# Optimization experiments

Measured on AMD Instinct MI355X. Metric: run time of the kernel, lower is better.

## Reference

```python
import jax, jax.numpy as jnp
import numpy as np

N_NODES = 32
GAT_OUT = 64
LSTM_H = 128
N_CLS = 4
NEG_SLOPE = 0.2


def setup_inputs() -> dict:
    key = jax.random.key(0)
    ks = jax.random.split(key, 12)
    B, T, E = 32, 512, 96
    F, H = GAT_OUT, LSTM_H
    s = 0.05
    return {
        "x_seq": jax.random.normal(ks[0], (B, T, N_NODES), jnp.float32),
        "edge_index": jax.random.randint(ks[1], (2, E), 0, N_NODES, jnp.int32),
        # GATConv params (heads=1): lin weight [in=1, F], attention vectors [F], bias [F]
        "w_gat": jax.random.normal(ks[2], (1, F), jnp.float32) * s,
        "att_src": jax.random.normal(ks[3], (F,), jnp.float32) * s,
        "att_dst": jax.random.normal(ks[4], (F,), jnp.float32) * s,
        "b_gat": jnp.zeros((F,), jnp.float32),
        # LSTM params, torch gate order (i, f, g, o)
        "W_ih": jax.random.normal(ks[5], (N_NODES * F, 4 * H), jnp.float32) * s,
        "W_hh": jax.random.normal(ks[6], (H, 4 * H), jnp.float32) * s,
        "b_ih": jnp.zeros((4 * H,), jnp.float32),
        "b_hh": jnp.zeros((4 * H,), jnp.float32),
        # classifier
        "W_fc": jax.random.normal(ks[7], (H, N_CLS), jnp.float32) * s,
        "b_fc": jnp.zeros((N_CLS,), jnp.float32),
    }


def _forward(x_seq, edge_index, w_gat, att_src, att_dst, b_gat,
             W_ih, W_hh, b_ih, b_hh, W_fc, b_fc):
    B, T, N = x_seq.shape
    F = w_gat.shape[1]
    H = W_hh.shape[0]

    # --- GAT over all (B,T) steps at once (PyG GATConv, heads=1, self-loops) ---
    loops = jnp.arange(N, dtype=edge_index.dtype)
    src = jnp.concatenate([edge_index[0], loops])  # [Et]
    dst = jnp.concatenate([edge_index[1], loops])  # [Et]
    Et = src.shape[0]

    h = x_seq[..., None] * w_gat            # [B,T,N,F] (in_channels=1 linear)
    a_s = h @ att_src                        # [B,T,N]
    a_d = h @ att_dst                        # [B,T,N]
    e = a_s[..., src] + a_d[..., dst]        # [B,T,Et]
    e = jnp.where(e > 0, e, NEG_SLOPE * e)   # LeakyReLU(0.2)

    # segment softmax over destination node, batched over B*T
    e2 = jnp.moveaxis(e, -1, 0).reshape(Et, B * T)
    m = jax.ops.segment_max(e2, dst, num_segments=N)        # [N,B*T]
    ex = jnp.exp(e2 - m[dst])
    z = jax.ops.segment_sum(ex, dst, num_segments=N)        # [N,B*T]
    alpha = ex / z[dst]                                      # [Et,B*T]
    alpha = jnp.moveaxis(alpha.reshape(Et, B, T), 0, -1)     # [B,T,Et]

    msg = alpha[..., None] * h[:, :, src, :]                 # [B,T,Et,F]
    onehot = (dst[:, None] == jnp.arange(N)).astype(h.dtype)  # [Et,N]
    out = jnp.einsum('btef,en->btnf', msg, onehot) + b_gat    # [B,T,N,F]

    seq = out.reshape(B, T, N * F)           # [B,T,2048]

    # --- single-layer LSTM (batch_first), torch gate order i,f,g,o ---
    xw = seq @ W_ih + (b_ih + b_hh)          # [B,T,4H]

    def step(carry, xw_t):
        hs, cs = carry
        g = xw_t + hs @ W_hh                 # [B,4H]
        i, f, gg, o = jnp.split(g, 4, axis=-1)
        cs = jax.nn.sigmoid(f) * cs + jax.nn.sigmoid(i) * jnp.tanh(gg)
        hs = jax.nn.sigmoid(o) * jnp.tanh(cs)
        return (hs, cs), None

    h0 = jnp.zeros((B, H), seq.dtype)
    (h_last, _), _ = jax.lax.scan(step, (h0, h0), jnp.moveaxis(xw, 1, 0))

    return h_last @ W_fc + b_fc              # [B,num_classes]


def reference(x_seq, edge_index, w_gat, att_src, att_dst, b_gat,
              W_ih, W_hh, b_ih, b_hh, W_fc, b_fc):
    return _forward(x_seq, edge_index, w_gat, att_src, att_dst, b_gat,
                    W_ih, W_hh, b_ih, b_hh, W_fc, b_fc)
```

## Files before the change

### kernel.cpp

```cpp
#include <hip/hip_runtime.h>

#define NN 32
#define FF 64
#define HH 128
#define G4 512
#define BB 32
#define TT 512
#define ET 128
#define NPOS (BB*TT)

__device__ __forceinline__ float frcp(float x) { return __builtin_amdgcn_rcpf(x); }

__global__ __launch_bounds__(512) void prep_kernel(const float* __restrict__ w_gat,
                                                   const float* __restrict__ b_gat,
                                                   const float* __restrict__ W_ih,
                                                   const float* __restrict__ W_hh,
                                                   float* __restrict__ W_eff,
                                                   float* __restrict__ biasp,
                                                   float* __restrict__ Wt) {
  int j = threadIdx.x;
  int n = blockIdx.x;
  float accw = 0.f, accb = 0.f;
#pragma unroll 8
  for (int f = 0; f < FF; ++f) {
    float wv = W_ih[(n * FF + f) * G4 + j];
    accw = fmaf(w_gat[f], wv, accw);
    accb = fmaf(b_gat[f], wv, accb);
  }
  W_eff[n * G4 + j] = accw;
  biasp[n * G4 + j] = accb;
  int g0 = (n * G4 + j) * 4;
#pragma unroll
  for (int q = 0; q < 4; ++q) {
    int E = g0 + q;
    int tl = E >> 7;
    int idx = E & 127;
    int s = idx >> 5;
    int jj = (idx >> 3) & 3;
    int g = (idx >> 1) & 3;
    int e = idx & 1;
    int r = tl >> 2, kq = tl & 3, lr = r & 3;
    int bb = (lr - s) & 3;
    int k = kq * 32 + 8 * bb + 2 * jj + e;
    Wt[E] = W_hh[k * G4 + g * 128 + r];
  }
}

__global__ __launch_bounds__(256) void gatxw_kernel(const float* __restrict__ x_seq,
                                                    const int* __restrict__ ei,
                                                    const float* __restrict__ w_gat,
                                                    const float* __restrict__ att_src,
                                                    const float* __restrict__ att_dst,
                                                    const float* __restrict__ b_ih,
                                                    const float* __restrict__ b_hh,
                                                    const float* __restrict__ W_eff,
                                                    const float* __restrict__ biasp,
                                                    float* __restrict__ xw) {
  __shared__ int srt[ET];
  __shared__ int offs[NN + 1];
  __shared__ int cnt[NN];
  __shared__ float xs[256];
  __shared__ float sl[256];
  __shared__ float scal_sh[2];
  int tid = threadIdx.x;
  int posbase = blockIdx.x * 8;
  float we0[NN], we1[NN];
#pragma unroll
  for (int nn = 0; nn < NN; ++nn) {
    we0[nn] = W_eff[nn * G4 + tid];
    we1[nn] = W_eff[nn * G4 + 256 + tid];
  }
  float b0 = b_ih[tid] + b_hh[tid];
  float b1 = b_ih[256 + tid] + b_hh[256 + tid];
#pragma unroll 8
  for (int n = 0; n < NN; ++n) {
    b0 += biasp[n * G4 + tid];
    b1 += biasp[n * G4 + 256 + tid];
  }
  if (tid < NN) cnt[tid] = 0;
  __syncthreads();
  int es = 0, ed = 0, tk = 0;
  if (tid < ET) {
    if (tid < 96) { es = ei[tid]; ed = ei[96 + tid]; }
    else { es = tid - 96; ed = tid - 96; }
    tk = atomicAdd(&cnt[ed], 1);
  }
  __syncthreads();
  if (tid == 0) {
    offs[0] = 0;
    for (int n = 0; n < NN; ++n) offs[n + 1] = offs[n] + cnt[n];
  }
  if (tid == 1) {
    float cs = 0.f, cd = 0.f;
    for (int f = 0; f < FF; ++f) {
      cs = fmaf(w_gat[f], att_src[f], cs);
      cd = fmaf(w_gat[f], att_dst[f], cd);
    }
    scal_sh[0] = cs;
    scal_sh[1] = cd;
  }
  __syncthreads();
  if (tid < ET) srt[offs[ed] + tk] = es;
  xs[tid] = x_seq[posbase * NN + tid];
  __syncthreads();
  float cs = scal_sh[0], cd = scal_sh[1];
  int p = tid >> 5, n = tid & 31;
  int base = p * 32;
  int e0 = offs[n], e1 = offs[n + 1];
  float xn = xs[base + n];
  float cdxn = cd * xn;
  float m = -3.0e38f;
  for (int e = e0; e < e1; ++e) {
    float ev = fmaf(cs, xs[base + srt[e]], cdxn);
    ev = ev > 0.f ? ev : 0.2f * ev;
    m = fmaxf(m, ev);
  }
  float z = 0.f, sa = 0.f;
  for (int e = e0; e < e1; ++e) {
    float xsv = xs[base + srt[e]];
    float ev = fmaf(cs, xsv, cdxn);
    ev = ev > 0.f ? ev : 0.2f * ev;
    float ex = __expf(ev - m);
    z += ex;
    sa = fmaf(ex, xsv, sa);
  }
  sl[p * 32 + n] = sa * frcp(z);
  __syncthreads();
  for (int pp = 0; pp < 8; ++pp) {
    const float4* sp = (const float4*)&sl[pp * 32];
    float a0 = b0, a1 = b1;
#pragma unroll
    for (int q = 0; q < 8; ++q) {
      float4 sv = sp[q];
      a0 = fmaf(sv.x, we0[4 * q], a0);
      a0 = fmaf(sv.y, we0[4 * q + 1], a0);
      a0 = fmaf(sv.z, we0[4 * q + 2], a0);
      a0 = fmaf(sv.w, we0[4 * q + 3], a0);
      a1 = fmaf(sv.x, we1[4 * q], a1);
      a1 = fmaf(sv.y, we1[4 * q + 1], a1);
      a1 = fmaf(sv.z, we1[4 * q + 2], a1);
      a1 = fmaf(sv.w, we1[4 * q + 3], a1);
    }
    size_t row = (size_t)(posbase + pp) * G4;
    xw[row + tid] = a0;
    xw[row + 256 + tid] = a1;
  }
}


#define PK4F(HP, W0, W1, W2, W3) \
  "v_pk_fma_f32 v[216:217], v[" HP "], v[" W0 "], 0\n\t" \
  "v_pk_fma_f32 v[218:219], v[" HP "], v[" W1 "], 0\n\t" \
  "v_pk_fma_f32 v[220:221], v[" HP "], v[" W2 "], 0\n\t" \
  "v_pk_fma_f32 v[222:223], v[" HP "], v[" W3 "], 0\n\t"

#define PK4A(HP, W0, W1, W2, W3) \
  "v_pk_fma_f32 v[216:217], v[" HP "], v[" W0 "], v[216:217]\n\t" \
  "v_pk_fma_f32 v[218:219], v[" HP "], v[" W1 "], v[218:219]\n\t" \
  "v_pk_fma_f32 v[220:221], v[" HP "], v[" W2 "], v[220:221]\n\t" \
  "v_pk_fma_f32 v[222:223], v[" HP "], v[" W3 "], v[222:223]\n\t"

#define ROT8 \
  "v_mov_b32_dpp v32, v32 row_ror:4 row_mask:0xf bank_mask:0xf\n\t" \
  "v_mov_b32_dpp v33, v33 row_ror:4 row_mask:0xf bank_mask:0xf\n\t" \
  "v_mov_b32_dpp v34, v34 row_ror:4 row_mask:0xf bank_mask:0xf\n\t" \
  "v_mov_b32_dpp v35, v35 row_ror:4 row_mask:0xf bank_mask:0xf\n\t" \
  "v_mov_b32_dpp v36, v36 row_ror:4 row_mask:0xf bank_mask:0xf\n\t" \
  "v_mov_b32_dpp v37, v37 row_ror:4 row_mask:0xf bank_mask:0xf\n\t" \
  "v_mov_b32_dpp v38, v38 row_ror:4 row_mask:0xf bank_mask:0xf\n\t" \
  "v_mov_b32_dpp v39, v39 row_ror:4 row_mask:0xf bank_mask:0xf\n\t"

#define PHASE(XSLOT, RD, WR) \
  "ds_read_b128 v[32:35], " RD "\n\t" \
  "ds_read_b128 v[36:39], " RD " offset:16\n\t" \
  "s_waitcnt lgkmcnt(1)\n\t" \
  PK4F("32:33", "64:65",   "66:67",   "68:69",   "70:71") \
  PK4A("34:35", "72:73",   "74:75",   "76:77",   "78:79") \
  "s_waitcnt lgkmcnt(0)\n\t" \
  PK4A("36:37", "80:81",   "82:83",   "84:85",   "86:87") \
  PK4A("38:39", "88:89",   "90:91",   "92:93",   "94:95") \
  ROT8 \
  PK4A("32:33", "96:97",   "98:99",   "100:101", "102:103") \
  PK4A("34:35", "104:105", "106:107", "108:109", "110:111") \
  PK4A("36:37", "112:113", "114:115", "116:117", "118:119") \
  PK4A("38:39", "120:121", "122:123", "124:125", "126:127") \
  ROT8 \
  PK4A("32:33", "128:129", "130:131", "132:133", "134:135") \
  PK4A("34:35", "136:137", "138:139", "140:141", "142:143") \
  PK4A("36:37", "144:145", "146:147", "148:149", "150:151") \
  PK4A("38:39", "152:153", "154:155", "156:157", "158:159") \
  ROT8 \
  PK4A("32:33", "160:161", "162:163", "164:165", "166:167") \
  PK4A("34:35", "168:169", "170:171", "172:173", "174:175") \
  PK4A("36:37", "176:177", "178:179", "180:181", "182:183") \
  PK4A("38:39", "184:185", "186:187", "188:189", "190:191") \
  "s_waitcnt vmcnt(3)\n\t" \
  "v_mov_b32 v215, " XSLOT "\n\t" \
  "global_load_dword " XSLOT ", v194, %[xwb]\n\t" \
  "v_add_u32 v194, 0x800, v194\n\t" \
  "v_add_f32 v204, v216, v217\n\t" \
  "v_add_f32 v205, v218, v219\n\t" \
  "v_add_f32 v206, v220, v221\n\t" \
  "v_add_f32 v207, v222, v223\n\t" \
  "v_add_f32_dpp v204, v204, v204 quad_perm:[1,0,3,2] row_mask:0xf bank_mask:0xf\n\t" \
  "v_add_f32_dpp v205, v205, v205 quad_perm:[1,0,3,2] row_mask:0xf bank_mask:0xf\n\t" \
  "v_add_f32_dpp v206, v206, v206 quad_perm:[1,0,3,2] row_mask:0xf bank_mask:0xf\n\t" \
  "v_add_f32_dpp v207, v207, v207 quad_perm:[1,0,3,2] row_mask:0xf bank_mask:0xf\n\t" \
  "v_add_f32_dpp v204, v204, v204 quad_perm:[2,3,0,1] row_mask:0xf bank_mask:0xf\n\t" \
  "v_add_f32_dpp v205, v205, v205 quad_perm:[2,3,0,1] row_mask:0xf bank_mask:0xf\n\t" \
  "v_add_f32_dpp v206, v206, v206 quad_perm:[2,3,0,1] row_mask:0xf bank_mask:0xf\n\t" \
  "v_add_f32_dpp v207, v207, v207 quad_perm:[2,3,0,1] row_mask:0xf bank_mask:0xf\n\t" \
  "v_cndmask_b32 v208, v204, v205, s[22:23]\n\t" \
  "v_cndmask_b32 v209, v206, v207, s[22:23]\n\t" \
  "v_cndmask_b32 v208, v208, v209, s[24:25]\n\t" \
  "v_add_f32 v208, v208, v215\n\t" \
  "v_mul_f32 v209, v200, v208\n\t" \
  "v_exp_f32 v209, v209\n\t" \
  "s_nop 0\n\t" \
  "v_add_f32 v209, 1.0, v209\n\t" \
  "v_rcp_f32 v209, v209\n\t" \
  "s_nop 0\n\t" \
  "v_fma_f32 v210, v201, v209, v202\n\t" \
  "s_nop 1\n\t" \
  "v_add_f32_dpp v211, v210, v203 quad_perm:[0,0,0,0] row_mask:0xf bank_mask:0xf\n\t" \
  "v_add_f32_dpp v212, v210, v203 quad_perm:[1,1,1,1] row_mask:0xf bank_mask:0xf\n\t" \
  "v_add_f32_dpp v213, v210, v203 quad_perm:[2,2,2,2] row_mask:0xf bank_mask:0xf\n\t" \
  "v_add_f32_dpp v214, v210, v203 quad_perm:[3,3,3,3] row_mask:0xf bank_mask:0xf\n\t" \
  "v_mul_f32 v211, v211, v213\n\t" \
  "v_fma_f32 v199, v212, v199, v211\n\t" \
  "v_mul_f32 v209, 0x4038aa3b, v199\n\t" \
  "v_exp_f32 v209, v209\n\t" \
  "s_nop 0\n\t" \
  "v_add_f32 v209, 1.0, v209\n\t" \
  "v_rcp_f32 v209, v209\n\t" \
  "s_nop 0\n\t" \
  "v_fma_f32 v209, -2.0, v209, 1.0\n\t" \
  "v_mul_f32 v209, v214, v209\n\t" \
  "ds_write_b32 " WR ", v209\n\t" \
  "s_waitcnt lgkmcnt(0)\n\t" \
  "s_barrier\n\t"

__global__ __launch_bounds__(512, 2) void lstm_kernel(const float* __restrict__ xw,
                                                      const float* __restrict__ Wt,
                                                      const float* __restrict__ W_fc,
                                                      const float* __restrict__ b_fc,
                                                      float* __restrict__ out) {
  __shared__ __align__(16) float lds[256];
  int b = blockIdx.x, tid = threadIdx.x;
  int r = tid >> 2, kq = tid & 3;
  int lr = r & 3;
  if (tid < 256) lds[tid] = 0.f;
  const float* xwb = xw + (size_t)b * TT * G4;
  unsigned xoff0 = (unsigned)((kq * 128 + r) * 4);
  unsigned wtoff = (unsigned)(tid * 512);
  unsigned lbase = (unsigned)(uintptr_t)&lds[0];
  unsigned rda = lbase + (unsigned)(kq * 128 + lr * 32);
  unsigned rdb = rda + 512;
  unsigned wra = lbase + (unsigned)(r * 4);
  unsigned wrb = wra + 512;
  float kmulf = (kq == 2) ? __uint_as_float(0x4038aa3bu)
                          : __uint_as_float(0xbfb8aa3bu);
  float Af = (kq == 2) ? -2.f : 1.f;
  float Bf = (kq == 2) ? 1.f : 0.f;
  unsigned kqodd = kq & 1, kqhi = kq >> 1;
  __syncthreads();
  asm volatile(
    "v_mov_b32 v194, %[xo]\n\t"
    "v_mov_b32 v195, %[rda]\n\t"
    "v_mov_b32 v196, %[rdb]\n\t"
    "v_mov_b32 v197, %[wra]\n\t"
    "v_mov_b32 v198, %[wrb]\n\t"
    "v_mov_b32 v199, 0\n\t"
    "v_mov_b32 v200, %[km]\n\t"
    "v_mov_b32 v201, %[Aa]\n\t"
    "v_mov_b32 v202, %[Bb]\n\t"
    "v_mov_b32 v203, 0\n\t"
    "v_cmp_eq_u32 s[22:23], 1, %[kodd]\n\t"
    "v_cmp_eq_u32 s[24:25], 1, %[khi]\n\t"
    "global_load_dword v224, v194, %[xwb]\n\t"
    "v_add_u32 v194, 0x800, v194\n\t"
    "global_load_dword v225, v194, %[xwb]\n\t"
    "v_add_u32 v194, 0x800, v194\n\t"
    "global_load_dword v226, v194, %[xwb]\n\t"
    "v_add_u32 v194, 0x800, v194\n\t"
    "global_load_dword v227, v194, %[xwb]\n\t"
    "v_add_u32 v194, 0x800, v194\n\t"
    "global_load_dwordx4 v[64:67], %[wto], %[wtb] offset:0\n\t"
    "global_load_dwordx4 v[68:71], %[wto], %[wtb] offset:16\n\t"
    "global_load_dwordx4 v[72:75], %[wto], %[wtb] offset:32\n\t"
    "global_load_dwordx4 v[76:79], %[wto], %[wtb] offset:48\n\t"
    "global_load_dwordx4 v[80:83], %[wto], %[wtb] offset:64\n\t"
    "global_load_dwordx4 v[84:87], %[wto], %[wtb] offset:80\n\t"
    "global_load_dwordx4 v[88:91], %[wto], %[wtb] offset:96\n\t"
    "global_load_dwordx4 v[92:95], %[wto], %[wtb] offset:112\n\t"
    "global_load_dwordx4 v[96:99], %[wto], %[wtb] offset:128\n\t"
    "global_load_dwordx4 v[100:103], %[wto], %[wtb] offset:144\n\t"
    "global_load_dwordx4 v[104:107], %[wto], %[wtb] offset:160\n\t"
    "global_load_dwordx4 v[108:111], %[wto], %[wtb] offset:176\n\t"
    "global_load_dwordx4 v[112:115], %[wto], %[wtb] offset:192\n\t"
    "global_load_dwordx4 v[116:119], %[wto], %[wtb] offset:208\n\t"
    "global_load_dwordx4 v[120:123], %[wto], %[wtb] offset:224\n\t"
    "global_load_dwordx4 v[124:127], %[wto], %[wtb] offset:240\n\t"
    "global_load_dwordx4 v[128:131], %[wto], %[wtb] offset:256\n\t"
    "global_load_dwordx4 v[132:135], %[wto], %[wtb] offset:272\n\t"
    "global_load_dwordx4 v[136:139], %[wto], %[wtb] offset:288\n\t"
    "global_load_dwordx4 v[140:143], %[wto], %[wtb] offset:304\n\t"
    "global_load_dwordx4 v[144:147], %[wto], %[wtb] offset:320\n\t"
    "global_load_dwordx4 v[148:151], %[wto], %[wtb] offset:336\n\t"
    "global_load_dwordx4 v[152:155], %[wto], %[wtb] offset:352\n\t"
    "global_load_dwordx4 v[156:159], %[wto], %[wtb] offset:368\n\t"
    "global_load_dwordx4 v[160:163], %[wto], %[wtb] offset:384\n\t"
    "global_load_dwordx4 v[164:167], %[wto], %[wtb] offset:400\n\t"
    "global_load_dwordx4 v[168:171], %[wto], %[wtb] offset:416\n\t"
    "global_load_dwordx4 v[172:175], %[wto], %[wtb] offset:432\n\t"
    "global_load_dwordx4 v[176:179], %[wto], %[wtb] offset:448\n\t"
    "global_load_dwordx4 v[180:183], %[wto], %[wtb] offset:464\n\t"
    "global_load_dwordx4 v[184:187], %[wto], %[wtb] offset:480\n\t"
    "global_load_dwordx4 v[188:191], %[wto], %[wtb] offset:496\n\t"
    "s_waitcnt vmcnt(0)\n\t"
    "s_movk_i32 s20, 0x80\n\t"
    "L_lstm_%=:\n\t"
    PHASE("v224", "v195", "v198")
    PHASE("v225", "v196", "v197")
    PHASE("v226", "v195", "v198")
    PHASE("v227", "v196", "v197")
    "s_sub_u32 s20, s20, 1\n\t"
    "s_cmp_lg_u32 s20, 0\n\t"
    "s_cbranch_scc1 L_lstm_%=\n\t"
    "s_waitcnt vmcnt(0) lgkmcnt(0)\n\t"
    :
    : [xwb]"s"(xwb), [wtb]"s"(Wt), [wto]"v"(wtoff), [xo]"v"(xoff0),
      [rda]"v"(rda), [rdb]"v"(rdb), [wra]"v"(wra), [wrb]"v"(wrb),
      [km]"v"(kmulf), [Aa]"v"(Af), [Bb]"v"(Bf),
      [kodd]"v"(kqodd), [khi]"v"(kqhi)
    : "memory", "scc", "s20", "s22", "s23", "s24", "s25",
      "v32","v33","v34","v35","v36","v37","v38","v39",
      "v40","v41","v42","v43","v44","v45","v46","v47",
      "v48","v49","v50","v51","v52","v53","v54","v55",
      "v56","v57","v58","v59","v60","v61","v62","v63",
      "v64","v65","v66","v67","v68","v69","v70","v71",
      "v72","v73","v74","v75","v76","v77","v78","v79",
      "v80","v81","v82","v83","v84","v85","v86","v87",
      "v88","v89","v90","v91","v92","v93","v94","v95",
      "v96","v97","v98","v99","v100","v101","v102","v103",
      "v104","v105","v106","v107","v108","v109","v110","v111",
      "v112","v113","v114","v115","v116","v117","v118","v119",
      "v120","v121","v122","v123","v124","v125","v126","v127",
      "v128","v129","v130","v131","v132","v133","v134","v135",
      "v136","v137","v138","v139","v140","v141","v142","v143",
      "v144","v145","v146","v147","v148","v149","v150","v151",
      "v152","v153","v154","v155","v156","v157","v158","v159",
      "v160","v161","v162","v163","v164","v165","v166","v167",
      "v168","v169","v170","v171","v172","v173","v174","v175",
      "v176","v177","v178","v179","v180","v181","v182","v183",
      "v184","v185","v186","v187","v188","v189","v190","v191",
      "v192","v193","v194","v195","v196","v197","v198","v199",
      "v200","v201","v202","v203","v204","v205","v206","v207",
      "v208","v209","v210","v211","v212","v213","v214","v215",
      "v216","v217","v218","v219","v220","v221","v222","v223",
      "v224","v225","v226","v227");
  __syncthreads();
  if (tid < 4) {
    float acc = b_fc[tid];
#pragma unroll 8
    for (int k = 0; k < HH; ++k)
      acc = fmaf(lds[k], W_fc[k * 4 + tid], acc);
    out[b * 4 + tid] = acc;
  }
}

extern "C" void kernel_launch(void* const* d_in, const int* in_sizes, int n_in,
                              void* d_out, int out_size, void* d_ws, size_t ws_size,
                              hipStream_t stream) {
  const float* x_seq   = (const float*)d_in[0];
  const int*   ei      = (const int*)d_in[1];
  const float* w_gat   = (const float*)d_in[2];
  const float* att_src = (const float*)d_in[3];
  const float* att_dst = (const float*)d_in[4];
  const float* b_gat   = (const float*)d_in[5];
  const float* W_ih    = (const float*)d_in[6];
  const float* W_hh    = (const float*)d_in[7];
  const float* b_ih    = (const float*)d_in[8];
  const float* b_hh    = (const float*)d_in[9];
  const float* W_fc    = (const float*)d_in[10];
  const float* b_fc    = (const float*)d_in[11];

  float* ws = (float*)d_ws;
  float* Wt    = ws;
  float* xw    = Wt + 65536;
  float* W_eff = xw + (size_t)(NPOS + 8) * G4;
  float* biasp = W_eff + NN * G4;

  prep_kernel<<<NN, G4, 0, stream>>>(w_gat, b_gat, W_ih, W_hh, W_eff, biasp, Wt);
  gatxw_kernel<<<NPOS / 8, 256, 0, stream>>>(x_seq, ei, w_gat, att_src, att_dst,
                                             b_ih, b_hh, W_eff, biasp, xw);
  lstm_kernel<<<BB, 512, 0, stream>>>(xw, Wt, W_fc, b_fc, (float*)d_out);
}
```

Measured before the change: 412.4 us.

## Split LSTM recurrence across 1024 threads with 8-way k-split per hidden unit

The LSTM kernel moves from 512 to 1024 threads per batch row. Each hidden unit's gate dot products are now split over 8 lanes of 16 k each instead of 4 lanes of 32. This halves the per-thread W_hh register footprint and the FMA chain per step, and replaces the DPP rotation scheme with direct LDS reads at fixed offsets. An extra row_half_mirror reduction stage is added. Gate activation now uses the same sigmoid/tanh trick with the lane-select done via shared multipliers. The cost is more waves per barrier, an added reduction step and redundant activation work per lane group.

```diff
diff --git a/kernel.cpp b/kernel.cpp
--- a/kernel.cpp
+++ b/kernel.cpp
@@ -31,17 +31,16 @@
   biasp[n * G4 + j] = accb;
   int g0 = (n * G4 + j) * 4;
 #pragma unroll
-  for (int q = 0; q < 4; ++q) {
-    int E = g0 + q;
-    int tl = E >> 7;
-    int idx = E & 127;
-    int s = idx >> 5;
-    int jj = (idx >> 3) & 3;
+  for (int qq = 0; qq < 4; ++qq) {
+    int E = g0 + qq;
+    int tl = E >> 6;
+    int idx = E & 63;
+    int cn = idx >> 4;
+    int p = (idx >> 3) & 1;
     int g = (idx >> 1) & 3;
     int e = idx & 1;
-    int r = tl >> 2, kq = tl & 3, lr = r & 3;
-    int bb = (lr - s) & 3;
-    int k = kq * 32 + 8 * bb + 2 * jj + e;
+    int r = tl >> 3, q = tl & 7;
+    int k = q * 16 + 4 * cn + 2 * p + e;
     Wt[E] = W_hh[k * G4 + g * 128 + r];
   }
 }
@@ -149,190 +148,147 @@
 
 
 #define PK4F(HP, W0, W1, W2, W3) \
-  "v_pk_fma_f32 v[216:217], v[" HP "], v[" W0 "], 0\n\t" \
-  "v_pk_fma_f32 v[218:219], v[" HP "], v[" W1 "], 0\n\t" \
-  "v_pk_fma_f32 v[220:221], v[" HP "], v[" W2 "], 0\n\t" \
-  "v_pk_fma_f32 v[222:223], v[" HP "], v[" W3 "], 0\n\t"
+  "v_pk_fma_f32 v[104:105], v[" HP "], v[" W0 "], 0\n\t" \
+  "v_pk_fma_f32 v[106:107], v[" HP "], v[" W1 "], 0\n\t" \
+  "v_pk_fma_f32 v[108:109], v[" HP "], v[" W2 "], 0\n\t" \
+  "v_pk_fma_f32 v[110:111], v[" HP "], v[" W3 "], 0\n\t"
 
 #define PK4A(HP, W0, W1, W2, W3) \
-  "v_pk_fma_f32 v[216:217], v[" HP "], v[" W0 "], v[216:217]\n\t" \
-  "v_pk_fma_f32 v[218:219], v[" HP "], v[" W1 "], v[218:219]\n\t" \
-  "v_pk_fma_f32 v[220:221], v[" HP "], v[" W2 "], v[220:221]\n\t" \
-  "v_pk_fma_f32 v[222:223], v[" HP "], v[" W3 "], v[222:223]\n\t"
-
-#define ROT8 \
-  "v_mov_b32_dpp v32, v32 row_ror:4 row_mask:0xf bank_mask:0xf\n\t" \
-  "v_mov_b32_dpp v33, v33 row_ror:4 row_mask:0xf bank_mask:0xf\n\t" \
-  "v_mov_b32_dpp v34, v34 row_ror:4 row_mask:0xf bank_mask:0xf\n\t" \
-  "v_mov_b32_dpp v35, v35 row_ror:4 row_mask:0xf bank_mask:0xf\n\t" \
-  "v_mov_b32_dpp v36, v36 row_ror:4 row_mask:0xf bank_mask:0xf\n\t" \
-  "v_mov_b32_dpp v37, v37 row_ror:4 row_mask:0xf bank_mask:0xf\n\t" \
-  "v_mov_b32_dpp v38, v38 row_ror:4 row_mask:0xf bank_mask:0xf\n\t" \
-  "v_mov_b32_dpp v39, v39 row_ror:4 row_mask:0xf bank_mask:0xf\n\t"
-
-#define PHASE(XSLOT, RD, WR) \
-  "ds_read_b128 v[32:35], " RD "\n\t" \
-  "ds_read_b128 v[36:39], " RD " offset:16\n\t" \
+  "v_pk_fma_f32 v[104:105], v[" HP "], v[" W0 "], v[104:105]\n\t" \
+  "v_pk_fma_f32 v[106:107], v[" HP "], v[" W1 "], v[106:107]\n\t" \
+  "v_pk_fma_f32 v[108:109], v[" HP "], v[" W2 "], v[108:109]\n\t" \
+  "v_pk_fma_f32 v[110:111], v[" HP "], v[" W3 "], v[110:111]\n\t"
+
+#define PHASE(XSLOT, O0, O1, O2, O3, WOFF) \
+  "ds_read_b128 v[32:35], v124 offset:" O0 "\n\t" \
+  "ds_read_b128 v[36:39], v124 offset:" O1 "\n\t" \
   "s_waitcnt lgkmcnt(1)\n\t" \
-  PK4F("32:33", "64:65",   "66:67",   "68:69",   "70:71") \
-  PK4A("34:35", "72:73",   "74:75",   "76:77",   "78:79") \
+  PK4F("32:33", "40:41", "42:43", "44:45", "46:47") \
+  PK4A("34:35", "48:49", "50:51", "52:53", "54:55") \
+  "ds_read_b128 v[32:35], v124 offset:" O2 "\n\t" \
+  "s_waitcnt lgkmcnt(1)\n\t" \
+  PK4A("36:37", "56:57", "58:59", "60:61", "62:63") \
+  PK4A("38:39", "64:65", "66:67", "68:69", "70:71") \
+  "ds_read_b128 v[36:39], v124 offset:" O3 "\n\t" \
+  "s_waitcnt lgkmcnt(1)\n\t" \
+  PK4A("32:33", "72:73", "74:75", "76:77", "78:79") \
+  PK4A("34:35", "80:81", "82:83", "84:85", "86:87") \
   "s_waitcnt lgkmcnt(0)\n\t" \
-  PK4A("36:37", "80:81",   "82:83",   "84:85",   "86:87") \
-  PK4A("38:39", "88:89",   "90:91",   "92:93",   "94:95") \
-  ROT8 \
-  PK4A("32:33", "96:97",   "98:99",   "100:101", "102:103") \
-  PK4A("34:35", "104:105", "106:107", "108:109", "110:111") \
-  PK4A("36:37", "112:113", "114:115", "116:117", "118:119") \
-  PK4A("38:39", "120:121", "122:123", "124:125", "126:127") \
-  ROT8 \
-  PK4A("32:33", "128:129", "130:131", "132:133", "134:135") \
-  PK4A("34:35", "136:137", "138:139", "140:141", "142:143") \
-  PK4A("36:37", "144:145", "146:147", "148:149", "150:151") \
-  PK4A("38:39", "152:153", "154:155", "156:157", "158:159") \
-  ROT8 \
-  PK4A("32:33", "160:161", "162:163", "164:165", "166:167") \
-  PK4A("34:35", "168:169", "170:171", "172:173", "174:175") \
-  PK4A("36:37", "176:177", "178:179", "180:181", "182:183") \
-  PK4A("38:39", "184:185", "186:187", "188:189", "190:191") \
-  "s_waitcnt vmcnt(3)\n\t" \
-  "v_mov_b32 v215, " XSLOT "\n\t" \
-  "global_load_dword " XSLOT ", v194, %[xwb]\n\t" \
-  "v_add_u32 v194, 0x800, v194\n\t" \
-  "v_add_f32 v204, v216, v217\n\t" \
-  "v_add_f32 v205, v218, v219\n\t" \
-  "v_add_f32 v206, v220, v221\n\t" \
-  "v_add_f32 v207, v222, v223\n\t" \
-  "v_add_f32_dpp v204, v204, v204 quad_perm:[1,0,3,2] row_mask:0xf bank_mask:0xf\n\t" \
-  "v_add_f32_dpp v205, v205, v205 quad_perm:[1,0,3,2] row_mask:0xf bank_mask:0xf\n\t" \
-  "v_add_f32_dpp v206, v206, v206 quad_perm:[1,0,3,2] row_mask:0xf bank_mask:0xf\n\t" \
-  "v_add_f32_dpp v207, v207, v207 quad_perm:[1,0,3,2] row_mask:0xf bank_mask:0xf\n\t" \
-  "v_add_f32_dpp v204, v204, v204 quad_perm:[2,3,0,1] row_mask:0xf bank_mask:0xf\n\t" \
-  "v_add_f32_dpp v205, v205, v205 quad_perm:[2,3,0,1] row_mask:0xf bank_mask:0xf\n\t" \
-  "v_add_f32_dpp v206, v206, v206 quad_perm:[2,3,0,1] row_mask:0xf bank_mask:0xf\n\t" \
-  "v_add_f32_dpp v207, v207, v207 quad_perm:[2,3,0,1] row_mask:0xf bank_mask:0xf\n\t" \
-  "v_cndmask_b32 v208, v204, v205, s[22:23]\n\t" \
-  "v_cndmask_b32 v209, v206, v207, s[22:23]\n\t" \
-  "v_cndmask_b32 v208, v208, v209, s[24:25]\n\t" \
-  "v_add_f32 v208, v208, v215\n\t" \
-  "v_mul_f32 v209, v200, v208\n\t" \
-  "v_exp_f32 v209, v209\n\t" \
+  PK4A("36:37", "88:89", "90:91", "92:93", "94:95") \
+  PK4A("38:39", "96:97", "98:99", "100:101", "102:103") \
+  "v_add_f32 v112, v104, v105\n\t" \
+  "v_add_f32 v113, v106, v107\n\t" \
+  "v_add_f32 v114, v108, v109\n\t" \
+  "v_add_f32 v115, v110, v111\n\t" \
+  "v_add_f32_dpp v112, v112, v112 quad_perm:[1,0,3,2] row_mask:0xf bank_mask:0xf\n\t" \
+  "v_add_f32_dpp v113, v113, v113 quad_perm:[1,0,3,2] row_mask:0xf bank_mask:0xf\n\t" \
+  "v_add_f32_dpp v114, v114, v114 quad_perm:[1,0,3,2] row_mask:0xf bank_mask:0xf\n\t" \
+  "v_add_f32_dpp v115, v115, v115 quad_perm:[1,0,3,2] row_mask:0xf bank_mask:0xf\n\t" \
+  "v_add_f32_dpp v112, v112, v112 quad_perm:[2,3,0,1] row_mask:0xf bank_mask:0xf\n\t" \
+  "v_add_f32_dpp v113, v113, v113 quad_perm:[2,3,0,1] row_mask:0xf bank_mask:0xf\n\t" \
+  "v_add_f32_dpp v114, v114, v114 quad_perm:[2,3,0,1] row_mask:0xf bank_mask:0xf\n\t" \
+  "v_add_f32_dpp v115, v115, v115 quad_perm:[2,3,0,1] row_mask:0xf bank_mask:0xf\n\t" \
+  "v_add_f32_dpp v112, v112, v112 row_half_mirror row_mask:0xf bank_mask:0xf\n\t" \
+  "v_add_f32_dpp v113, v113, v113 row_half_mirror row_mask:0xf bank_mask:0xf\n\t" \
+  "v_add_f32_dpp v114, v114, v114 row_half_mirror row_mask:0xf bank_mask:0xf\n\t" \
+  "v_add_f32_dpp v115, v115, v115 row_half_mirror row_mask:0xf bank_mask:0xf\n\t" \
+  "v_cndmask_b32 v116, v112, v113, s[22:23]\n\t" \
+  "v_cndmask_b32 v117, v114, v115, s[22:23]\n\t" \
+  "v_cndmask_b32 v116, v116, v117, s[24:25]\n\t" \
+  "s_waitcnt vmcnt(1)\n\t" \
+  "v_add_f32 v116, v116, " XSLOT "\n\t" \
+  "global_load_dword " XSLOT ", v123, %[xwb]\n\t" \
+  "v_add_u32 v123, 0x800, v123\n\t" \
+  "v_mul_f32 v117, 0xbfb8aa3b, v116\n\t" \
+  "v_mul_f32 v117, v126, v117\n\t" \
+  "v_exp_f32 v117, v117\n\t" \
   "s_nop 0\n\t" \
-  "v_add_f32 v209, 1.0, v209\n\t" \
-  "v_rcp_f32 v209, v209\n\t" \
+  "v_add_f32 v117, 1.0, v117\n\t" \
+  "v_rcp_f32 v117, v117\n\t" \
   "s_nop 0\n\t" \
-  "v_fma_f32 v210, v201, v209, v202\n\t" \
+  "v_fma_f32 v118, v126, v117, v127\n\t" \
   "s_nop 1\n\t" \
-  "v_add_f32_dpp v211, v210, v203 quad_perm:[0,0,0,0] row_mask:0xf bank_mask:0xf\n\t" \
-  "v_add_f32_dpp v212, v210, v203 quad_perm:[1,1,1,1] row_mask:0xf bank_mask:0xf\n\t" \
-  "v_add_f32_dpp v213, v210, v203 quad_perm:[2,2,2,2] row_mask:0xf bank_mask:0xf\n\t" \
-  "v_add_f32_dpp v214, v210, v203 quad_perm:[3,3,3,3] row_mask:0xf bank_mask:0xf\n\t" \
-  "v_mul_f32 v211, v211, v213\n\t" \
-  "v_fma_f32 v199, v212, v199, v211\n\t" \
-  "v_mul_f32 v209, 0x4038aa3b, v199\n\t" \
-  "v_exp_f32 v209, v209\n\t" \
+  "v_mov_b32_dpp v112, v118 quad_perm:[0,0,0,0] row_mask:0xf bank_mask:0xf\n\t" \
+  "v_mov_b32_dpp v113, v118 quad_perm:[1,1,1,1] row_mask:0xf bank_mask:0xf\n\t" \
+  "v_mov_b32_dpp v114, v118 quad_perm:[2,2,2,2] row_mask:0xf bank_mask:0xf\n\t" \
+  "v_mov_b32_dpp v115, v118 quad_perm:[3,3,3,3] row_mask:0xf bank_mask:0xf\n\t" \
+  "v_mul_f32 v112, v112, v114\n\t" \
+  "v_fma_f32 v120, v113, v120, v112\n\t" \
+  "v_mul_f32 v117, 0x4038aa3b, v120\n\t" \
+  "v_exp_f32 v117, v117\n\t" \
   "s_nop 0\n\t" \
-  "v_add_f32 v209, 1.0, v209\n\t" \
-  "v_rcp_f32 v209, v209\n\t" \
+  "v_add_f32 v117, 1.0, v117\n\t" \
+  "v_rcp_f32 v117, v117\n\t" \
   "s_nop 0\n\t" \
-  "v_fma_f32 v209, -2.0, v209, 1.0\n\t" \
-  "v_mul_f32 v209, v214, v209\n\t" \
-  "ds_write_b32 " WR ", v209\n\t" \
+  "v_fma_f32 v117, -2.0, v117, 1.0\n\t" \
+  "v_mul_f32 v118, v115, v117\n\t" \
+  "ds_write_b32 v125, v118 offset:" WOFF "\n\t" \
   "s_waitcnt lgkmcnt(0)\n\t" \
   "s_barrier\n\t"
 
-__global__ __launch_bounds__(512, 2) void lstm_kernel(const float* __restrict__ xw,
-                                                      const float* __restrict__ Wt,
-                                                      const float* __restrict__ W_fc,
-                                                      const float* __restrict__ b_fc,
-                                                      float* __restrict__ out) {
+__global__ __launch_bounds__(1024, 4) void lstm_kernel(const float* __restrict__ xw,
+                                                       const float* __restrict__ Wt,
+                                                       const float* __restrict__ W_fc,
+                                                       const float* __restrict__ b_fc,
+                                                       float* __restrict__ out) {
   __shared__ __align__(16) float lds[256];
   int b = blockIdx.x, tid = threadIdx.x;
-  int r = tid >> 2, kq = tid & 3;
-  int lr = r & 3;
+  int r = tid >> 3, q = tid & 7;
+  int gq = q & 3;
   if (tid < 256) lds[tid] = 0.f;
   const float* xwb = xw + (size_t)b * TT * G4;
-  unsigned xoff0 = (unsigned)((kq * 128 + r) * 4);
-  unsigned wtoff = (unsigned)(tid * 512);
+  unsigned xoff0 = (unsigned)((gq * 128 + r) * 4);
+  unsigned wtoff = (unsigned)(tid * 256);
   unsigned lbase = (unsigned)(uintptr_t)&lds[0];
-  unsigned rda = lbase + (unsigned)(kq * 128 + lr * 32);
-  unsigned rdb = rda + 512;
-  unsigned wra = lbase + (unsigned)(r * 4);
-  unsigned wrb = wra + 512;
-  float kmulf = (kq == 2) ? __uint_as_float(0x4038aa3bu)
-                          : __uint_as_float(0xbfb8aa3bu);
-  float Af = (kq == 2) ? -2.f : 1.f;
-  float Bf = (kq == 2) ? 1.f : 0.f;
-  unsigned kqodd = kq & 1, kqhi = kq >> 1;
+  unsigned rd = lbase + (unsigned)(q * 64);
+  unsigned wr = lbase + (unsigned)(r * 4);
+  float Af = (gq == 2) ? -2.f : 1.f;
+  float Bf = (gq == 2) ? 1.f : 0.f;
+  unsigned qodd = q & 1, qhi = (q >> 1) & 1;
   __syncthreads();
   asm volatile(
-    "v_mov_b32 v194, %[xo]\n\t"
-    "v_mov_b32 v195, %[rda]\n\t"
-    "v_mov_b32 v196, %[rdb]\n\t"
-    "v_mov_b32 v197, %[wra]\n\t"
-    "v_mov_b32 v198, %[wrb]\n\t"
-    "v_mov_b32 v199, 0\n\t"
-    "v_mov_b32 v200, %[km]\n\t"
-    "v_mov_b32 v201, %[Aa]\n\t"
-    "v_mov_b32 v202, %[Bb]\n\t"
-    "v_mov_b32 v203, 0\n\t"
-    "v_cmp_eq_u32 s[22:23], 1, %[kodd]\n\t"
-    "v_cmp_eq_u32 s[24:25], 1, %[khi]\n\t"
-    "global_load_dword v224, v194, %[xwb]\n\t"
-    "v_add_u32 v194, 0x800, v194\n\t"
-    "global_load_dword v225, v194, %[xwb]\n\t"
-    "v_add_u32 v194, 0x800, v194\n\t"
-    "global_load_dword v226, v194, %[xwb]\n\t"
-    "v_add_u32 v194, 0x800, v194\n\t"
-    "global_load_dword v227, v194, %[xwb]\n\t"
-    "v_add_u32 v194, 0x800, v194\n\t"
-    "global_load_dwordx4 v[64:67], %[wto], %[wtb] offset:0\n\t"
-    "global_load_dwordx4 v[68:71], %[wto], %[wtb] offset:16\n\t"
-    "global_load_dwordx4 v[72:75], %[wto], %[wtb] offset:32\n\t"
-    "global_load_dwordx4 v[76:79], %[wto], %[wtb] offset:48\n\t"
-    "global_load_dwordx4 v[80:83], %[wto], %[wtb] offset:64\n\t"
-    "global_load_dwordx4 v[84:87], %[wto], %[wtb] offset:80\n\t"
-    "global_load_dwordx4 v[88:91], %[wto], %[wtb] offset:96\n\t"
-    "global_load_dwordx4 v[92:95], %[wto], %[wtb] offset:112\n\t"
-    "global_load_dwordx4 v[96:99], %[wto], %[wtb] offset:128\n\t"
-    "global_load_dwordx4 v[100:103], %[wto], %[wtb] offset:144\n\t"
-    "global_load_dwordx4 v[104:107], %[wto], %[wtb] offset:160\n\t"
-    "global_load_dwordx4 v[108:111], %[wto], %[wtb] offset:176\n\t"
-    "global_load_dwordx4 v[112:115], %[wto], %[wtb] offset:192\n\t"
-    "global_load_dwordx4 v[116:119], %[wto], %[wtb] offset:208\n\t"
-    "global_load_dwordx4 v[120:123], %[wto], %[wtb] offset:224\n\t"
-    "global_load_dwordx4 v[124:127], %[wto], %[wtb] offset:240\n\t"
-    "global_load_dwordx4 v[128:131], %[wto], %[wtb] offset:256\n\t"
-    "global_load_dwordx4 v[132:135], %[wto], %[wtb] offset:272\n\t"
-    "global_load_dwordx4 v[136:139], %[wto], %[wtb] offset:288\n\t"
-    "global_load_dwordx4 v[140:143], %[wto], %[wtb] offset:304\n\t"
-    "global_load_dwordx4 v[144:147], %[wto], %[wtb] offset:320\n\t"
-    "global_load_dwordx4 v[148:151], %[wto], %[wtb] offset:336\n\t"
-    "global_load_dwordx4 v[152:155], %[wto], %[wtb] offset:352\n\t"
-    "global_load_dwordx4 v[156:159], %[wto], %[wtb] offset:368\n\t"
-    "global_load_dwordx4 v[160:163], %[wto], %[wtb] offset:384\n\t"
-    "global_load_dwordx4 v[164:167], %[wto], %[wtb] offset:400\n\t"
-    "global_load_dwordx4 v[168:171], %[wto], %[wtb] offset:416\n\t"
-    "global_load_dwordx4 v[172:175], %[wto], %[wtb] offset:432\n\t"
-    "global_load_dwordx4 v[176:179], %[wto], %[wtb] offset:448\n\t"
-    "global_load_dwordx4 v[180:183], %[wto], %[wtb] offset:464\n\t"
-    "global_load_dwordx4 v[184:187], %[wto], %[wtb] offset:480\n\t"
-    "global_load_dwordx4 v[188:191], %[wto], %[wtb] offset:496\n\t"
+    "v_mov_b32 v123, %[xo]\n\t"
+    "v_mov_b32 v124, %[rd]\n\t"
+    "v_mov_b32 v125, %[wr]\n\t"
+    "v_mov_b32 v126, %[Aa]\n\t"
+    "v_mov_b32 v127, %[Bb]\n\t"
+    "v_mov_b32 v120, 0\n\t"
+    "v_cmp_eq_u32 s[22:23], 1, %[qodd]\n\t"
+    "v_cmp_eq_u32 s[24:25], 1, %[qhi]\n\t"
+    "global_load_dword v121, v123, %[xwb]\n\t"
+    "v_add_u32 v123, 0x800, v123\n\t"
+    "global_load_dword v122, v123, %[xwb]\n\t"
+    "v_add_u32 v123, 0x800, v123\n\t"
+    "global_load_dwordx4 v[40:43], %[wto], %[wtb] offset:0\n\t"
+    "global_load_dwordx4 v[44:47], %[wto], %[wtb] offset:16\n\t"
+    "global_load_dwordx4 v[48:51], %[wto], %[wtb] offset:32\n\t"
+    "global_load_dwordx4 v[52:55], %[wto], %[wtb] offset:48\n\t"
+    "global_load_dwordx4 v[56:59], %[wto], %[wtb] offset:64\n\t"
+    "global_load_dwordx4 v[60:63], %[wto], %[wtb] offset:80\n\t"
+    "global_load_dwordx4 v[64:67], %[wto], %[wtb] offset:96\n\t"
+    "global_load_dwordx4 v[68:71], %[wto], %[wtb] offset:112\n\t"
+    "global_load_dwordx4 v[72:75], %[wto], %[wtb] offset:128\n\t"
+    "global_load_dwordx4 v[76:79], %[wto], %[wtb] offset:144\n\t"
+    "global_load_dwordx4 v[80:83], %[wto], %[wtb] offset:160\n\t"
+    "global_load_dwordx4 v[84:87], %[wto], %[wtb] offset:176\n\t"
+    "global_load_dwordx4 v[88:91], %[wto], %[wtb] offset:192\n\t"
+    "global_load_dwordx4 v[92:95], %[wto], %[wtb] offset:208\n\t"
+    "global_load_dwordx4 v[96:99], %[wto], %[wtb] offset:224\n\t"
+    "global_load_dwordx4 v[100:103], %[wto], %[wtb] offset:240\n\t"
     "s_waitcnt vmcnt(0)\n\t"
-    "s_movk_i32 s20, 0x80\n\t"
+    "s_movk_i32 s20, 0x100\n\t"
     "L_lstm_%=:\n\t"
-    PHASE("v224", "v195", "v198")
-    PHASE("v225", "v196", "v197")
-    PHASE("v226", "v195", "v198")
-    PHASE("v227", "v196", "v197")
+    PHASE("v121", "0",   "16",  "32",  "48",  "512")
+    PHASE("v122", "512", "528", "544", "560", "0")
     "s_sub_u32 s20, s20, 1\n\t"
     "s_cmp_lg_u32 s20, 0\n\t"
     "s_cbranch_scc1 L_lstm_%=\n\t"
     "s_waitcnt vmcnt(0) lgkmcnt(0)\n\t"
     :
     : [xwb]"s"(xwb), [wtb]"s"(Wt), [wto]"v"(wtoff), [xo]"v"(xoff0),
-      [rda]"v"(rda), [rdb]"v"(rdb), [wra]"v"(wra), [wrb]"v"(wrb),
-      [km]"v"(kmulf), [Aa]"v"(Af), [Bb]"v"(Bf),
-      [kodd]"v"(kqodd), [khi]"v"(kqhi)
+      [rd]"v"(rd), [wr]"v"(wr),
+      [Aa]"v"(Af), [Bb]"v"(Bf),
+      [qodd]"v"(qodd), [qhi]"v"(qhi)
     : "memory", "scc", "s20", "s22", "s23", "s24", "s25",
       "v32","v33","v34","v35","v36","v37","v38","v39",
       "v40","v41","v42","v43","v44","v45","v46","v47",
@@ -345,20 +301,7 @@
       "v96","v97","v98","v99","v100","v101","v102","v103",
       "v104","v105","v106","v107","v108","v109","v110","v111",
       "v112","v113","v114","v115","v116","v117","v118","v119",
-      "v120","v121","v122","v123","v124","v125","v126","v127",
-      "v128","v129","v130","v131","v132","v133","v134","v135",
-      "v136","v137","v138","v139","v140","v141","v142","v143",
-      "v144","v145","v146","v147","v148","v149","v150","v151",
-      "v152","v153","v154","v155","v156","v157","v158","v159",
-      "v160","v161","v162","v163","v164","v165","v166","v167",
-      "v168","v169","v170","v171","v172","v173","v174","v175",
-      "v176","v177","v178","v179","v180","v181","v182","v183",
-      "v184","v185","v186","v187","v188","v189","v190","v191",
-      "v192","v193","v194","v195","v196","v197","v198","v199",
-      "v200","v201","v202","v203","v204","v205","v206","v207",
-      "v208","v209","v210","v211","v212","v213","v214","v215",
-      "v216","v217","v218","v219","v220","v221","v222","v223",
-      "v224","v225","v226","v227");
+      "v120","v121","v122","v123","v124","v125","v126","v127");
   __syncthreads();
   if (tid < 4) {
     float acc = b_fc[tid];
@@ -394,5 +337,5 @@
   prep_kernel<<<NN, G4, 0, stream>>>(w_gat, b_gat, W_ih, W_hh, W_eff, biasp, Wt);
   gatxw_kernel<<<NPOS / 8, 256, 0, stream>>>(x_seq, ei, w_gat, att_src, att_dst,
                                              b_ih, b_hh, W_eff, biasp, xw);
-  lstm_kernel<<<BB, 512, 0, stream>>>(xw, Wt, W_fc, b_fc, (float*)d_out);
+  lstm_kernel<<<BB, 1024, 0, stream>>>(xw, Wt, W_fc, b_fc, (float*)d_out);
 }
```

New measurement: 454.9 us. 1.1x slower.
